# Kernel optimization log

Measured on AMD Instinct MI355X. Metric: run time of the kernel, lower is better.

The kernel has to match this reference:

```python
import jax, jax.numpy as jnp
import numpy as np

D = 512
M_FUT = 3
EPS = 1e-12


def _lin(x, W, b):
    return x @ W + b


def _svd_orthogonalize(m):
    # m: [B, 9] -> [B, 3, 3] SO(3) via SVD orthogonalization (special Procrustes)
    m = m.reshape(-1, 3, 3)
    norm = jnp.maximum(jnp.linalg.norm(m, axis=-1, keepdims=True), EPS)
    mt = jnp.swapaxes(m / norm, -1, -2)          # normalize rows, then transpose
    u, s, vh = jnp.linalg.svd(mt, full_matrices=False)
    v = jnp.swapaxes(vh, -1, -2)                 # torch.svd returns V, jax returns V^H
    ut = jnp.swapaxes(u, -1, -2)
    det = jnp.linalg.det(jnp.matmul(v, ut))      # [B]
    v_adj = jnp.concatenate([v[:, :, :-1], v[:, :, -1:] * det[:, None, None]], axis=2)
    return jnp.matmul(v_adj, ut)


def setup_inputs() -> dict:
    key = jax.random.key(0)
    ks = iter(jax.random.split(key, 40))
    B, N, M = 32, 3, M_FUT
    ph = pw = 37
    BN, hw = B * N, ph * pw
    sc = 1.0 / np.sqrt(D)
    rn = lambda *shape: (jax.random.normal(next(ks), shape, dtype=jnp.float32) * sc)
    inp = {
        'feat': jax.random.normal(next(ks), (BN, hw, D), dtype=jnp.float32),
        'patch_h': ph, 'patch_w': pw, 'batch_size': B, 'num_current_frames': N,
        # two ResConvBlocks, three 512x512 Linears each (in==out -> skip is identity)
        'W_res': rn(2, 3, D, D), 'b_res': rn(2, 3, D),
        # TemporalCameraMLP
        'W_cur1': rn(D, D), 'b_cur1': rn(D), 'W_cur2': rn(D, D), 'b_cur2': rn(D),
        'W_tp1': rn(D, D), 'b_tp1': rn(D), 'W_tp2': rn(D, D * M), 'b_tp2': rn(D * M),
        'W_fut1': rn(D, D), 'b_fut1': rn(D), 'W_fut2': rn(D, D), 'b_fut2': rn(D),
        # more_mlps
        'W_m1': rn(D, D), 'b_m1': rn(D), 'W_m2': rn(D, D), 'b_m2': rn(D),
        # pose heads (fp32)
        'W_t': rn(D, 3), 'b_t': rn(3), 'W_r': rn(D, 9), 'b_r': rn(9),
    }
    return inp


def reference(feat, patch_h, patch_w, batch_size, num_current_frames,
              W_res, b_res, W_cur1, b_cur1, W_cur2, b_cur2,
              W_tp1, b_tp1, W_tp2, b_tp2, W_fut1, b_fut1, W_fut2, b_fut2,
              W_m1, b_m1, W_m2, b_m2, W_t, b_t, W_r, b_r):
    B, N = batch_size, num_current_frames
    M = W_tp2.shape[1] // W_tp2.shape[0]
    # stacked residual 1x1-conv (Linear) blocks
    for i in range(2):
        x = jax.nn.relu(_lin(feat, W_res[i, 0], b_res[i, 0]))
        x = jax.nn.relu(_lin(x, W_res[i, 1], b_res[i, 1]))
        x = jax.nn.relu(_lin(x, W_res[i, 2], b_res[i, 2]))
        feat = feat + x
    # AdaptiveAvgPool2d(1) over patch grid == mean over hw
    pooled = feat.mean(axis=1)                                  # [BN, D]
    # TemporalCameraMLP
    cur = _lin(jax.nn.relu(_lin(pooled, W_cur1, b_cur1)), W_cur2, b_cur2)   # [BN, D]
    gctx = pooled.reshape(B, N, -1).mean(axis=1)                            # [B, D]
    tf = _lin(jax.nn.relu(_lin(gctx, W_tp1, b_tp1)), W_tp2, b_tp2)          # [B, D*M]
    tf = tf.reshape(B * M, -1)
    fut = _lin(jax.nn.relu(_lin(tf, W_fut1, b_fut1)), W_fut2, b_fut2)       # [B*M, D]
    allf = jnp.concatenate([cur, fut], axis=0)                              # [B*(N+M), D]
    h = jax.nn.relu(_lin(jax.nn.relu(_lin(allf, W_m1, b_m1)), W_m2, b_m2))
    # pose head in fp32
    hf = h.astype(jnp.float32)
    out_t = _lin(hf, W_t, b_t)                                  # [newBN, 3]
    out_r = _lin(hf, W_r, b_r)                                  # [newBN, 9]
    r = _svd_orthogonalize(out_r)                               # [newBN, 3, 3]
    newBN = allf.shape[0]
    pose = jnp.zeros((newBN, 4, 4), dtype=jnp.float32)
    pose = pose.at[:, :3, :3].set(r)
    pose = pose.at[:, :3, 3].set(out_t)
    pose = pose.at[:, 3, 3].set(1.0)
    return pose
```

## Files before the change

### kernel.cpp

```cpp
#include <hip/hip_runtime.h>


typedef unsigned short u16;
typedef __attribute__((ext_vector_type(8))) short short8;
typedef __attribute__((ext_vector_type(4))) float f32x4;

constexpr int  DDIM    = 512;
constexpr long R_ROWS  = 96L * 1369L;
constexpr long R_PAD   = 1027L * 128L;
constexpr int  RT_GRID = 1032;

__device__ __forceinline__ u16 f2b(float f) {
  union { float f; unsigned u; } x; x.f = f;
  unsigned r = (x.u + 0x7FFFu + ((x.u >> 16) & 1u)) >> 16;
  return (u16)r;
}
__device__ __forceinline__ float b2f(u16 b) {
  union { unsigned u; float f; } x; x.u = ((unsigned)b) << 16;
  return x.f;
}

__global__ void convert_feat_k(const float* __restrict__ in, u16* __restrict__ out) {
  long i4 = ((long)blockIdx.x * 256 + threadIdx.x) * 4;
  if (i4 >= R_PAD * DDIM) return;
  ushort4 o;
  if (i4 < R_ROWS * DDIM) {
    float4 v = *(const float4*)(in + i4);
    o.x = f2b(v.x); o.y = f2b(v.y); o.z = f2b(v.z); o.w = f2b(v.w);
  } else {
    o.x = 0; o.y = 0; o.z = 0; o.w = 0;
  }
  *(ushort4*)(out + i4) = o;
}

__global__ void transpose_w_k(const float* __restrict__ W, u16* __restrict__ Wt) {
  int idx = blockIdx.x * 256 + threadIdx.x;
  if (idx >= 6 * 512 * 512) return;
  int g = idx >> 18, rem = idx & 262143;
  int n = rem >> 9, k = rem & 511;
  Wt[idx] = f2b(W[(long)g * 262144 + (long)k * 512 + n]);
}

template <int MODE>
__global__ __launch_bounds__(256, 4)
void gemm_k(const u16* __restrict__ X, const u16* __restrict__ Wt,
            const float* __restrict__ bias, const u16* Res, u16* Y) {
  __shared__ u16 lA[128 * 64];
  __shared__ u16 lB[128 * 64];
  const int tid  = threadIdx.x;
  const int lane = tid & 63;
  const int wv   = tid >> 6;
  const int wm   = wv & 1;
  const int wn   = wv >> 1;
  const int l15  = lane & 15;
  const int quad = lane >> 4;

  const int b   = blockIdx.x;
  const int win = b >> 5, i32 = b & 31;
  const int rt  = win * 8 + (i32 & 7);
  const int ct  = i32 >> 3;
  if (rt >= 1027) return;
  const int  colBase = ct * 128;
  const long rowBase = (long)rt * 128;

  f32x4 acc[4][4];
#pragma unroll
  for (int i = 0; i < 4; ++i)
#pragma unroll
    for (int j = 0; j < 4; ++j) acc[i][j] = (f32x4){0.f, 0.f, 0.f, 0.f};

  for (int k0 = 0; k0 < 512; k0 += 64) {
#pragma unroll
    for (int j = 0; j < 4; ++j) {
      int L = tid + 256 * j;
      int r = L >> 3, cS = L & 7;
      int c = cS ^ (r & 7);
      const u16* ga = X + (rowBase + r) * DDIM + (k0 + c * 8);
      __builtin_amdgcn_global_load_lds(
          (const __attribute__((address_space(1))) void*)ga,
          (__attribute__((address_space(3))) void*)&lA[L * 8], 16, 0, 0);
      const u16* gb = Wt + (long)(colBase + r) * DDIM + (k0 + c * 8);
      __builtin_amdgcn_global_load_lds(
          (const __attribute__((address_space(1))) void*)gb,
          (__attribute__((address_space(3))) void*)&lB[L * 8], 16, 0, 0);
    }
    __syncthreads();
#pragma unroll
    for (int kk = 0; kk < 2; ++kk) {
      const int cx = (((kk * 4 + quad) ^ (l15 & 7))) * 8;
      short8 af[4], bfr[4];
#pragma unroll
      for (int i = 0; i < 4; ++i)
        af[i] = *(const short8*)&lA[(wm * 64 + i * 16 + l15) * 64 + cx];
#pragma unroll
      for (int j = 0; j < 4; ++j)
        bfr[j] = *(const short8*)&lB[(wn * 64 + j * 16 + l15) * 64 + cx];
#pragma unroll
      for (int i = 0; i < 4; ++i)
#pragma unroll
        for (int j = 0; j < 4; ++j)
          acc[i][j] = __builtin_amdgcn_mfma_f32_16x16x32_bf16(af[i], bfr[j], acc[i][j], 0, 0, 0);
    }
    __syncthreads();
  }

#pragma unroll
  for (int j = 0; j < 4; ++j) {
    int col = colBase + wn * 64 + j * 16 + l15;
    float bv = bias[col];
#pragma unroll
    for (int i = 0; i < 4; ++i) {
      long row0 = rowBase + wm * 64 + i * 16 + quad * 4;
#pragma unroll
      for (int r = 0; r < 4; ++r) {
        float v = acc[i][j][r] + bv;
        v = fmaxf(v, 0.f);
        long idx = (row0 + r) * DDIM + col;
        if (MODE == 1) v += b2f(Res[idx]);
        Y[idx] = f2b(v);
      }
    }
  }
}

__global__ void zero_k(float* p, int n) {
  int i = blockIdx.x * 256 + threadIdx.x;
  if (i < n) p[i] = 0.f;
}

__global__ void pool_k(const u16* __restrict__ feat, float* __restrict__ pooled) {
  int bn = blockIdx.x, ch = blockIdx.y, d = threadIdx.x;
  int p0 = ch * 172, p1 = p0 + 172;
  if (p1 > 1369) p1 = 1369;
  float s = 0.f;
  long base = ((long)bn * 1369 + p0) * DDIM + d;
  for (int p = p0; p < p1; ++p) { s += b2f(feat[base]); base += DDIM; }
  atomicAdd(&pooled[bn * DDIM + d], s * (1.0f / 1369.0f));
}

__global__ void gctx_k(const float* __restrict__ pooled, float* __restrict__ gctx) {
  int i = blockIdx.x * 256 + threadIdx.x;
  if (i >= 32 * DDIM) return;
  int b = i >> 9, d = i & 511;
  const float* p = pooled + (long)b * 3 * DDIM + d;
  gctx[i] = (p[0] + p[DDIM] + p[2 * DDIM]) * (1.0f / 3.0f);
}

template <bool RELU>
__global__ void lin_k(const float* __restrict__ in, const float* __restrict__ W,
                      const float* __restrict__ bias, float* __restrict__ out,
                      int K, int N) {
  int n = blockIdx.x * 256 + threadIdx.x;
  int r = blockIdx.y;
  if (n >= N) return;
  float acc = bias[n];
  const float* xi = in + (long)r * K;
#pragma unroll 8
  for (int k = 0; k < K; ++k) acc = fmaf(xi[k], W[(long)k * N + n], acc);
  if (RELU) acc = fmaxf(acc, 0.f);
  out[(long)r * N + n] = acc;
}

__global__ void pose_k(const float* __restrict__ h,
                       const float* __restrict__ Wt, const float* __restrict__ bt,
                       const float* __restrict__ Wr, const float* __restrict__ br,
                       float* __restrict__ out) {
  int row = blockIdx.x;
  int lane = threadIdx.x;
  const float* hr = h + (long)row * DDIM;
  float part[12];
#pragma unroll
  for (int c = 0; c < 12; ++c) {
    float acc = 0.f;
    for (int k = lane; k < DDIM; k += 64) {
      float wvv = (c < 3) ? Wt[k * 3 + c] : Wr[k * 9 + (c - 3)];
      acc += hr[k] * wvv;
    }
#pragma unroll
    for (int off = 32; off > 0; off >>= 1) acc += __shfl_down(acc, off);
    part[c] = acc;
  }
  if (lane != 0) return;

  double t3[3];
  for (int i = 0; i < 3; ++i) t3[i] = (double)part[i] + (double)bt[i];
  double m[3][3];
  for (int i = 0; i < 3; ++i)
    for (int j = 0; j < 3; ++j) m[i][j] = (double)part[3 + i * 3 + j] + (double)br[i * 3 + j];
  for (int i = 0; i < 3; ++i) {
    double nn = sqrt(m[i][0] * m[i][0] + m[i][1] * m[i][1] + m[i][2] * m[i][2]);
    if (nn < 1e-12) nn = 1e-12;
    m[i][0] /= nn; m[i][1] /= nn; m[i][2] /= nn;
  }
  double Km[3][3];
  for (int a = 0; a < 3; ++a)
    for (int b = 0; b < 3; ++b) {
      double s = 0;
      for (int i = 0; i < 3; ++i) s += m[i][a] * m[i][b];
      Km[a][b] = s;
    }
  double V[3][3] = {{1, 0, 0}, {0, 1, 0}, {0, 0, 1}};
  const int PQ[3][2] = {{0, 1}, {0, 2}, {1, 2}};
  for (int sweep = 0; sweep < 20; ++sweep) {
    for (int e = 0; e < 3; ++e) {
      int p = PQ[e][0], q = PQ[e][1];
      double apq = Km[p][q];
      if (apq == 0.0) continue;
      double tau = (Km[q][q] - Km[p][p]) / (2.0 * apq);
      double tt = (tau >= 0.0 ? 1.0 : -1.0) / (fabs(tau) + sqrt(1.0 + tau * tau));
      double cc = 1.0 / sqrt(1.0 + tt * tt), ss = tt * cc;
      for (int k = 0; k < 3; ++k) { double a1 = Km[p][k], a2 = Km[q][k]; Km[p][k] = cc * a1 - ss * a2; Km[q][k] = ss * a1 + cc * a2; }
      for (int k = 0; k < 3; ++k) { double a1 = Km[k][p], a2 = Km[k][q]; Km[k][p] = cc * a1 - ss * a2; Km[k][q] = ss * a1 + cc * a2; }
      for (int k = 0; k < 3; ++k) { double a1 = V[k][p], a2 = V[k][q]; V[k][p] = cc * a1 - ss * a2; V[k][q] = ss * a1 + cc * a2; }
    }
  }
  double lam[3] = {Km[0][0], Km[1][1], Km[2][2]};
  int o0 = 0, o1 = 1, o2 = 2; double detV = 1.0;
  if (lam[o0] < lam[o1]) { int t = o0; o0 = o1; o1 = t; detV = -detV; }
  if (lam[o1] < lam[o2]) { int t = o1; o1 = o2; o2 = t; detV = -detV; }
  if (lam[o0] < lam[o1]) { int t = o0; o0 = o1; o1 = t; detV = -detV; }
  double v0[3] = {V[0][o0], V[1][o0], V[2][o0]};
  double v1[3] = {V[0][o1], V[1][o1], V[2][o1]};
  double v2[3] = {V[0][o2], V[1][o2], V[2][o2]};
  double u0[3], u1[3];
  for (int i = 0; i < 3; ++i) u0[i] = m[i][0] * v0[0] + m[i][1] * v0[1] + m[i][2] * v0[2];
  double n0 = sqrt(u0[0] * u0[0] + u0[1] * u0[1] + u0[2] * u0[2]); if (n0 < 1e-30) n0 = 1e-30;
  for (int i = 0; i < 3; ++i) u0[i] /= n0;
  for (int i = 0; i < 3; ++i) u1[i] = m[i][0] * v1[0] + m[i][1] * v1[1] + m[i][2] * v1[2];
  double d01 = u0[0] * u1[0] + u0[1] * u1[1] + u0[2] * u1[2];
  for (int i = 0; i < 3; ++i) u1[i] -= d01 * u0[i];
  double n1 = sqrt(u1[0] * u1[0] + u1[1] * u1[1] + u1[2] * u1[2]); if (n1 < 1e-30) n1 = 1e-30;
  for (int i = 0; i < 3; ++i) u1[i] /= n1;
  double u2[3] = {u0[1] * u1[2] - u0[2] * u1[1],
                  u0[2] * u1[0] - u0[0] * u1[2],
                  u0[0] * u1[1] - u0[1] * u1[0]};
  float* o = out + (long)row * 16;
  for (int i = 0; i < 3; ++i) {
    for (int j = 0; j < 3; ++j)
      o[i * 4 + j] = (float)(u0[i] * v0[j] + u1[i] * v1[j] + detV * u2[i] * v2[j]);
    o[i * 4 + 3] = (float)t3[i];
  }
  o[12] = 0.f; o[13] = 0.f; o[14] = 0.f; o[15] = 1.f;
}

extern "C" void kernel_launch(void* const* d_in, const int* in_sizes, int n_in,
                              void* d_out, int out_size, void* d_ws, size_t ws_size,
                              hipStream_t stream) {
  (void)in_sizes; (void)n_in; (void)out_size; (void)ws_size;
  const float* feat   = (const float*)d_in[0];
  const float* W_res  = (const float*)d_in[5];
  const float* b_res  = (const float*)d_in[6];
  const float* W_cur1 = (const float*)d_in[7];
  const float* b_cur1 = (const float*)d_in[8];
  const float* W_cur2 = (const float*)d_in[9];
  const float* b_cur2 = (const float*)d_in[10];
  const float* W_tp1  = (const float*)d_in[11];
  const float* b_tp1  = (const float*)d_in[12];
  const float* W_tp2  = (const float*)d_in[13];
  const float* b_tp2  = (const float*)d_in[14];
  const float* W_fut1 = (const float*)d_in[15];
  const float* b_fut1 = (const float*)d_in[16];
  const float* W_fut2 = (const float*)d_in[17];
  const float* b_fut2 = (const float*)d_in[18];
  const float* W_m1   = (const float*)d_in[19];
  const float* b_m1   = (const float*)d_in[20];
  const float* W_m2   = (const float*)d_in[21];
  const float* b_m2   = (const float*)d_in[22];
  const float* W_t    = (const float*)d_in[23];
  const float* b_t    = (const float*)d_in[24];
  const float* W_r    = (const float*)d_in[25];
  const float* b_r    = (const float*)d_in[26];

  char* ws = (char*)d_ws;
  const size_t SZ_BIG = (size_t)R_PAD * DDIM * 2;
  u16* A   = (u16*)(ws);
  u16* Bb  = (u16*)(ws + SZ_BIG);
  u16* Cb  = (u16*)(ws + 2 * SZ_BIG);
  u16* Wt6 = (u16*)(ws + 3 * SZ_BIG);
  char* tail = ws + 3 * SZ_BIG + (size_t)6 * 512 * 512 * 2;
  float* pooled = (float*)(tail);
  float* gctx   = pooled + 96 * 512;
  float* tmp    = gctx + 32 * 512;
  float* tfb    = tmp + 192 * 512;
  float* allf   = tfb + 32 * 1536;
  float* h2     = allf + 192 * 512;
  float* outp   = (float*)d_out;

  convert_feat_k<<<65728, 256, 0, stream>>>(feat, A);
  transpose_w_k<<<6144, 256, 0, stream>>>(W_res, Wt6);

  const int NB = RT_GRID * 4;
  const size_t WS1 = (size_t)512 * 512;
  gemm_k<0><<<NB, 256, 0, stream>>>(A,  Wt6 + 0 * WS1, b_res + 0 * 512, nullptr, Bb);
  gemm_k<0><<<NB, 256, 0, stream>>>(Bb, Wt6 + 1 * WS1, b_res + 1 * 512, nullptr, Cb);
  gemm_k<1><<<NB, 256, 0, stream>>>(Cb, Wt6 + 2 * WS1, b_res + 2 * 512, A, A);
  gemm_k<0><<<NB, 256, 0, stream>>>(A,  Wt6 + 3 * WS1, b_res + 3 * 512, nullptr, Bb);
  gemm_k<0><<<NB, 256, 0, stream>>>(Bb, Wt6 + 4 * WS1, b_res + 4 * 512, nullptr, Cb);
  gemm_k<1><<<NB, 256, 0, stream>>>(Cb, Wt6 + 5 * WS1, b_res + 5 * 512, A, A);

  zero_k<<<(96 * 512 + 255) / 256, 256, 0, stream>>>(pooled, 96 * 512);
  pool_k<<<dim3(96, 8), 512, 0, stream>>>(A, pooled);
  gctx_k<<<(32 * 512 + 255) / 256, 256, 0, stream>>>(pooled, gctx);

  lin_k<true ><<<dim3(2, 96),  256, 0, stream>>>(pooled, W_cur1, b_cur1, tmp, 512, 512);
  lin_k<false><<<dim3(2, 96),  256, 0, stream>>>(tmp, W_cur2, b_cur2, allf, 512, 512);
  lin_k<true ><<<dim3(2, 32),  256, 0, stream>>>(gctx, W_tp1, b_tp1, tmp, 512, 512);
  lin_k<false><<<dim3(6, 32),  256, 0, stream>>>(tmp, W_tp2, b_tp2, tfb, 512, 1536);
  lin_k<true ><<<dim3(2, 96),  256, 0, stream>>>(tfb, W_fut1, b_fut1, tmp, 512, 512);
  lin_k<false><<<dim3(2, 96),  256, 0, stream>>>(tmp, W_fut2, b_fut2, allf + 96 * 512, 512, 512);
  lin_k<true ><<<dim3(2, 192), 256, 0, stream>>>(allf, W_m1, b_m1, tmp, 512, 512);
  lin_k<true ><<<dim3(2, 192), 256, 0, stream>>>(tmp, W_m2, b_m2, h2, 512, 512);

  pose_k<<<192, 64, 0, stream>>>(h2, W_t, b_t, W_r, b_r, outp);
}
```

Before: 1.634 ms.

## Double-buffer GEMM LDS tiles and stage epilogue through LDS for vector stores

Splits the GEMM main loop into two LDS buffers so the global-to-LDS loads for the next K slice are issued while MFMAs run on the current slice, with one barrier per iteration. The epilogue now writes bias+ReLU results into a swizzled fp32 LDS tile, then reads them back row-contiguously so the residual read and the bf16 output store become 16-byte vector accesses instead of scattered 2-byte ones. LDS use grows to 64 KB per block and launch bounds drop to 2 waves per SIMD, which cuts occupancy.

```diff
diff --git a/kernel.cpp b/kernel.cpp
--- a/kernel.cpp
+++ b/kernel.cpp
@@ -18,6 +18,10 @@
 __device__ __forceinline__ float b2f(u16 b) {
   union { unsigned u; float f; } x; x.u = ((unsigned)b) << 16;
   return x.f;
+}
+
+__device__ __forceinline__ int csw(int row, int col) {
+  return col ^ (((col >> 5) & 3) << 2) ^ (((row >> 2) & 1) << 4);
 }
 
 __global__ void convert_feat_k(const float* __restrict__ in, u16* __restrict__ out) {
@@ -42,11 +46,14 @@
 }
 
 template <int MODE>
-__global__ __launch_bounds__(256, 4)
+__global__ __launch_bounds__(256, 2)
 void gemm_k(const u16* __restrict__ X, const u16* __restrict__ Wt,
             const float* __restrict__ bias, const u16* Res, u16* Y) {
-  __shared__ u16 lA[128 * 64];
-  __shared__ u16 lB[128 * 64];
+  __shared__ __align__(16) char smem[65536];
+  u16 (*lA)[128 * 64] = reinterpret_cast<u16(*)[128 * 64]>(smem);
+  u16 (*lB)[128 * 64] = reinterpret_cast<u16(*)[128 * 64]>(smem + 32768);
+  float* lC = reinterpret_cast<float*>(smem);
+
   const int tid  = threadIdx.x;
   const int lane = tid & 63;
   const int wv   = tid >> 6;
@@ -69,7 +76,7 @@
 #pragma unroll
     for (int j = 0; j < 4; ++j) acc[i][j] = (f32x4){0.f, 0.f, 0.f, 0.f};
 
-  for (int k0 = 0; k0 < 512; k0 += 64) {
+  auto STAGE = [&](int p, int k0) {
 #pragma unroll
     for (int j = 0; j < 4; ++j) {
       int L = tid + 256 * j;
@@ -78,23 +85,30 @@
       const u16* ga = X + (rowBase + r) * DDIM + (k0 + c * 8);
       __builtin_amdgcn_global_load_lds(
           (const __attribute__((address_space(1))) void*)ga,
-          (__attribute__((address_space(3))) void*)&lA[L * 8], 16, 0, 0);
+          (__attribute__((address_space(3))) void*)&lA[p][L * 8], 16, 0, 0);
       const u16* gb = Wt + (long)(colBase + r) * DDIM + (k0 + c * 8);
       __builtin_amdgcn_global_load_lds(
           (const __attribute__((address_space(1))) void*)gb,
-          (__attribute__((address_space(3))) void*)&lB[L * 8], 16, 0, 0);
-    }
-    __syncthreads();
+          (__attribute__((address_space(3))) void*)&lB[p][L * 8], 16, 0, 0);
+    }
+  };
+
+  STAGE(0, 0);
+  __syncthreads();
+
+  int p = 0;
+  for (int t = 0; t < 8; ++t) {
+    if (t < 7) STAGE(p ^ 1, (t + 1) * 64);
 #pragma unroll
     for (int kk = 0; kk < 2; ++kk) {
       const int cx = (((kk * 4 + quad) ^ (l15 & 7))) * 8;
       short8 af[4], bfr[4];
 #pragma unroll
       for (int i = 0; i < 4; ++i)
-        af[i] = *(const short8*)&lA[(wm * 64 + i * 16 + l15) * 64 + cx];
+        af[i] = *(const short8*)&lA[p][(wm * 64 + i * 16 + l15) * 64 + cx];
 #pragma unroll
       for (int j = 0; j < 4; ++j)
-        bfr[j] = *(const short8*)&lB[(wn * 64 + j * 16 + l15) * 64 + cx];
+        bfr[j] = *(const short8*)&lB[p][(wn * 64 + j * 16 + l15) * 64 + cx];
 #pragma unroll
       for (int i = 0; i < 4; ++i)
 #pragma unroll
@@ -102,24 +116,43 @@
           acc[i][j] = __builtin_amdgcn_mfma_f32_16x16x32_bf16(af[i], bfr[j], acc[i][j], 0, 0, 0);
     }
     __syncthreads();
+    p ^= 1;
   }
 
 #pragma unroll
   for (int j = 0; j < 4; ++j) {
-    int col = colBase + wn * 64 + j * 16 + l15;
-    float bv = bias[col];
+    int colj = wn * 64 + j * 16 + l15;
+    float bv = bias[colBase + colj];
 #pragma unroll
     for (int i = 0; i < 4; ++i) {
-      long row0 = rowBase + wm * 64 + i * 16 + quad * 4;
+      int row0 = wm * 64 + i * 16 + quad * 4;
 #pragma unroll
       for (int r = 0; r < 4; ++r) {
-        float v = acc[i][j][r] + bv;
-        v = fmaxf(v, 0.f);
-        long idx = (row0 + r) * DDIM + col;
-        if (MODE == 1) v += b2f(Res[idx]);
-        Y[idx] = f2b(v);
+        int row = row0 + r;
+        lC[row * 128 + csw(row, colj)] = fmaxf(acc[i][j][r] + bv, 0.f);
       }
     }
+  }
+  __syncthreads();
+
+#pragma unroll
+  for (int it = 0; it < 8; ++it) {
+    int idx = it * 256 + tid;
+    int row = idx >> 4;
+    int c8  = (idx & 15) * 8;
+    float v[8];
+    *(float4*)&v[0] = *(const float4*)&lC[row * 128 + csw(row, c8)];
+    *(float4*)&v[4] = *(const float4*)&lC[row * 128 + csw(row, c8 + 4)];
+    long gidx = (rowBase + row) * DDIM + colBase + c8;
+    if (MODE == 1) {
+      short8 rv = *(const short8*)&Res[gidx];
+#pragma unroll
+      for (int k = 0; k < 8; ++k) v[k] += b2f((u16)rv[k]);
+    }
+    short8 o;
+#pragma unroll
+    for (int k = 0; k < 8; ++k) o[k] = (short)f2b(v[k]);
+    *(short8*)&Y[gidx] = o;
   }
 }
 
```

After: 1.467 ms. 1.11x faster.

## Fuse three residual-block GEMMs into one kernel keeping activations in LDS

Applied to the files above, without the earlier changes.

Replaces the six separate tiled GEMM launches with two fused kernels. Each block keeps a 64-row activation tile (all 512 columns) resident in shared memory across the three Linear layers and adds the residual in the epilogue. Weights are streamed straight from global memory into registers with one-step prefetch instead of being staged through LDS. This removes the intermediate global round-trips of the Bb and Cb activation buffers, but relies on L2 for the weight reads, uses 64 KB of LDS per block, and reduces the M tile to 64 rows.

```diff
diff --git a/kernel.cpp b/kernel.cpp
--- a/kernel.cpp
+++ b/kernel.cpp
@@ -7,8 +7,7 @@
 
 constexpr int  DDIM    = 512;
 constexpr long R_ROWS  = 96L * 1369L;
-constexpr long R_PAD   = 1027L * 128L;
-constexpr int  RT_GRID = 1032;
+constexpr long R_PAD   = 2054L * 64L;
 
 __device__ __forceinline__ u16 f2b(float f) {
   union { float f; unsigned u; } x; x.f = f;
@@ -41,83 +40,122 @@
   Wt[idx] = f2b(W[(long)g * 262144 + (long)k * 512 + n]);
 }
 
-template <int MODE>
-__global__ __launch_bounds__(256, 4)
-void gemm_k(const u16* __restrict__ X, const u16* __restrict__ Wt,
-            const float* __restrict__ bias, const u16* Res, u16* Y) {
-  __shared__ u16 lA[128 * 64];
-  __shared__ u16 lB[128 * 64];
+__global__ __launch_bounds__(512, 2)
+void fused_res_k(u16* __restrict__ A, const u16* __restrict__ Wt3,
+                 const float* __restrict__ bias3) {
+  __shared__ __align__(16) u16 S[64 * 512];
+  float* S32 = (float*)S;
   const int tid  = threadIdx.x;
   const int lane = tid & 63;
-  const int wv   = tid >> 6;
-  const int wm   = wv & 1;
-  const int wn   = wv >> 1;
+  const int wn   = tid >> 6;
   const int l15  = lane & 15;
   const int quad = lane >> 4;
-
-  const int b   = blockIdx.x;
-  const int win = b >> 5, i32 = b & 31;
-  const int rt  = win * 8 + (i32 & 7);
-  const int ct  = i32 >> 3;
-  if (rt >= 1027) return;
-  const int  colBase = ct * 128;
-  const long rowBase = (long)rt * 128;
-
-  f32x4 acc[4][4];
-#pragma unroll
-  for (int i = 0; i < 4; ++i)
-#pragma unroll
-    for (int j = 0; j < 4; ++j) acc[i][j] = (f32x4){0.f, 0.f, 0.f, 0.f};
-
-  for (int k0 = 0; k0 < 512; k0 += 64) {
-#pragma unroll
-    for (int j = 0; j < 4; ++j) {
-      int L = tid + 256 * j;
-      int r = L >> 3, cS = L & 7;
-      int c = cS ^ (r & 7);
-      const u16* ga = X + (rowBase + r) * DDIM + (k0 + c * 8);
-      __builtin_amdgcn_global_load_lds(
-          (const __attribute__((address_space(1))) void*)ga,
-          (__attribute__((address_space(3))) void*)&lA[L * 8], 16, 0, 0);
-      const u16* gb = Wt + (long)(colBase + r) * DDIM + (k0 + c * 8);
-      __builtin_amdgcn_global_load_lds(
-          (const __attribute__((address_space(1))) void*)gb,
-          (__attribute__((address_space(3))) void*)&lB[L * 8], 16, 0, 0);
-    }
+  const long rowBase = (long)blockIdx.x * 64;
+
+#pragma unroll
+  for (int j = 0; j < 8; ++j) {
+    int L = tid + 512 * j;
+    int r = L >> 6, cS = L & 63;
+    int c = cS ^ (r & 7);
+    const u16* ga = A + (rowBase + r) * DDIM + c * 8;
+    __builtin_amdgcn_global_load_lds(
+        (const __attribute__((address_space(1))) void*)ga,
+        (__attribute__((address_space(3))) void*)&S[L * 8], 16, 0, 0);
+  }
+  __syncthreads();
+
+  for (int layer = 0; layer < 3; ++layer) {
+    const u16*  W    = Wt3 + (long)layer * 262144;
+    const float* bias = bias3 + layer * 512;
+
+    f32x4 acc[4][4];
+#pragma unroll
+    for (int i = 0; i < 4; ++i)
+#pragma unroll
+      for (int j = 0; j < 4; ++j) acc[i][j] = (f32x4){0.f, 0.f, 0.f, 0.f};
+
+    const u16* wb = W + (long)(wn * 64 + l15) * DDIM + quad * 8;
+    short8 bf[4], bfN[4];
+#pragma unroll
+    for (int j = 0; j < 4; ++j) bf[j] = *(const short8*)(wb + j * 16 * DDIM);
+
+#pragma unroll
+    for (int kk = 0; kk < 16; ++kk) {
+      if (kk < 15) {
+#pragma unroll
+        for (int j = 0; j < 4; ++j)
+          bfN[j] = *(const short8*)(wb + j * 16 * DDIM + (kk + 1) * 32);
+      }
+      short8 af[4];
+      const int slot = ((kk * 4 + quad) ^ (l15 & 7)) * 8;
+#pragma unroll
+      for (int i = 0; i < 4; ++i)
+        af[i] = *(const short8*)&S[(i * 16 + l15) * DDIM + slot];
+#pragma unroll
+      for (int i = 0; i < 4; ++i)
+#pragma unroll
+        for (int j = 0; j < 4; ++j)
+          acc[i][j] = __builtin_amdgcn_mfma_f32_16x16x32_bf16(af[i], bf[j], acc[i][j], 0, 0, 0);
+      if (kk < 15) {
+#pragma unroll
+        for (int j = 0; j < 4; ++j) bf[j] = bfN[j];
+      }
+    }
+
     __syncthreads();
-#pragma unroll
-    for (int kk = 0; kk < 2; ++kk) {
-      const int cx = (((kk * 4 + quad) ^ (l15 & 7))) * 8;
-      short8 af[4], bfr[4];
+
+    float bv[4];
+#pragma unroll
+    for (int j = 0; j < 4; ++j) bv[j] = bias[wn * 64 + j * 16 + l15];
+
+    if (layer < 2) {
 #pragma unroll
       for (int i = 0; i < 4; ++i)
-        af[i] = *(const short8*)&lA[(wm * 64 + i * 16 + l15) * 64 + cx];
-#pragma unroll
-      for (int j = 0; j < 4; ++j)
-        bfr[j] = *(const short8*)&lB[(wn * 64 + j * 16 + l15) * 64 + cx];
-#pragma unroll
-      for (int i = 0; i < 4; ++i)
-#pragma unroll
-        for (int j = 0; j < 4; ++j)
-          acc[i][j] = __builtin_amdgcn_mfma_f32_16x16x32_bf16(af[i], bfr[j], acc[i][j], 0, 0, 0);
-    }
-    __syncthreads();
-  }
-
-#pragma unroll
-  for (int j = 0; j < 4; ++j) {
-    int col = colBase + wn * 64 + j * 16 + l15;
-    float bv = bias[col];
-#pragma unroll
-    for (int i = 0; i < 4; ++i) {
-      long row0 = rowBase + wm * 64 + i * 16 + quad * 4;
-#pragma unroll
-      for (int r = 0; r < 4; ++r) {
-        float v = acc[i][j][r] + bv;
-        v = fmaxf(v, 0.f);
-        long idx = (row0 + r) * DDIM + col;
-        if (MODE == 1) v += b2f(Res[idx]);
-        Y[idx] = f2b(v);
+#pragma unroll
+        for (int j = 0; j < 4; ++j) {
+          int col = wn * 64 + j * 16 + l15;
+#pragma unroll
+          for (int r = 0; r < 4; ++r) {
+            int row = i * 16 + quad * 4 + r;
+            float v = fmaxf(acc[i][j][r] + bv[j], 0.f);
+            S[row * DDIM + (((col >> 3) ^ (row & 7)) << 3) + (col & 7)] = f2b(v);
+          }
+        }
+      __syncthreads();
+    } else {
+#pragma unroll
+      for (int h = 0; h < 2; ++h) {
+#pragma unroll
+        for (int i2 = 0; i2 < 2; ++i2) {
+          int i = h * 2 + i2;
+#pragma unroll
+          for (int j = 0; j < 4; ++j) {
+            int col = wn * 64 + j * 16 + l15;
+#pragma unroll
+            for (int r = 0; r < 4; ++r) {
+              int row = i * 16 + quad * 4 + r;
+              int rl  = row - h * 32;
+              float v = fmaxf(acc[i][j][r] + bv[j], 0.f);
+              S32[rl * DDIM + (((col >> 2) ^ (rl & 7)) << 2) + (col & 3)] = v;
+            }
+          }
+        }
+        __syncthreads();
+#pragma unroll
+        for (int it = 0; it < 4; ++it) {
+          int idx = it * 512 + tid;
+          int r = idx >> 6, c = idx & 63;
+          float4 va = *(const float4*)&S32[r * DDIM + ((((2 * c)     ^ (r & 7))) << 2)];
+          float4 vb = *(const float4*)&S32[r * DDIM + ((((2 * c + 1) ^ (r & 7))) << 2)];
+          long g = (rowBase + h * 32 + r) * DDIM + c * 8;
+          short8 xv = *(const short8*)&A[g];
+          float vv[8] = {va.x, va.y, va.z, va.w, vb.x, vb.y, vb.z, vb.w};
+          short8 o;
+#pragma unroll
+          for (int k = 0; k < 8; ++k) o[k] = (short)f2b(vv[k] + b2f((u16)xv[k]));
+          *(short8*)&A[g] = o;
+        }
+        __syncthreads();
       }
     }
   }
@@ -274,8 +312,6 @@
   char* ws = (char*)d_ws;
   const size_t SZ_BIG = (size_t)R_PAD * DDIM * 2;
   u16* A   = (u16*)(ws);
-  u16* Bb  = (u16*)(ws + SZ_BIG);
-  u16* Cb  = (u16*)(ws + 2 * SZ_BIG);
   u16* Wt6 = (u16*)(ws + 3 * SZ_BIG);
   char* tail = ws + 3 * SZ_BIG + (size_t)6 * 512 * 512 * 2;
   float* pooled = (float*)(tail);
@@ -289,14 +325,9 @@
   convert_feat_k<<<65728, 256, 0, stream>>>(feat, A);
   transpose_w_k<<<6144, 256, 0, stream>>>(W_res, Wt6);
 
-  const int NB = RT_GRID * 4;
   const size_t WS1 = (size_t)512 * 512;
-  gemm_k<0><<<NB, 256, 0, stream>>>(A,  Wt6 + 0 * WS1, b_res + 0 * 512, nullptr, Bb);
-  gemm_k<0><<<NB, 256, 0, stream>>>(Bb, Wt6 + 1 * WS1, b_res + 1 * 512, nullptr, Cb);
-  gemm_k<1><<<NB, 256, 0, stream>>>(Cb, Wt6 + 2 * WS1, b_res + 2 * 512, A, A);
-  gemm_k<0><<<NB, 256, 0, stream>>>(A,  Wt6 + 3 * WS1, b_res + 3 * 512, nullptr, Bb);
-  gemm_k<0><<<NB, 256, 0, stream>>>(Bb, Wt6 + 4 * WS1, b_res + 4 * 512, nullptr, Cb);
-  gemm_k<1><<<NB, 256, 0, stream>>>(Cb, Wt6 + 5 * WS1, b_res + 5 * 512, A, A);
+  fused_res_k<<<2054, 512, 0, stream>>>(A, Wt6,           b_res);
+  fused_res_k<<<2054, 512, 0, stream>>>(A, Wt6 + 3 * WS1, b_res + 3 * 512);
 
   zero_k<<<(96 * 512 + 255) / 256, 256, 0, stream>>>(pooled, 96 * 512);
   pool_k<<<dim3(96, 8), 512, 0, stream>>>(A, pooled);
```

Measured after the change: 1.772 ms. +8.4%, slower.
